# Kernel tuning notes

Measured on AMD Instinct MI355X. Metric: run time of the kernel, lower is better.

## Reference

```python
import jax, jax.numpy as jnp
import numpy as np

B, S, D = 1, 2048, 2048
H, KVH = 32, 8
HD = D // H          # 64
N_REP = H // KVH     # 4
ROPE_THETA = 10000.0
NEG = -1e9


def setup_inputs() -> dict:
    key = jax.random.key(0)
    ks = jax.random.split(key, 8)
    x = jax.random.normal(ks[0], (B, S, D), dtype=jnp.float32)
    # RoPE tables: freqs_cis[t, j] = exp(i * t * theta^{-2j/HD}), j in [0, HD/2)
    inv_freq = 1.0 / (ROPE_THETA ** (jnp.arange(0, HD, 2, dtype=jnp.float32) / HD))
    angles = jnp.arange(S, dtype=jnp.float32)[:, None] * inv_freq[None, :]  # (S, HD/2)
    freqs_cos = jnp.cos(angles)
    freqs_sin = jnp.sin(angles)
    # causal additive mask (S, S)
    mask = jnp.where(jnp.tril(jnp.ones((S, S), dtype=bool)), 0.0, NEG).astype(jnp.float32)
    sc = 0.02
    wq = jax.random.normal(ks[1], (D, H * HD), dtype=jnp.float32) * sc
    wk = jax.random.normal(ks[2], (D, KVH * HD), dtype=jnp.float32) * sc
    wv = jax.random.normal(ks[3], (D, KVH * HD), dtype=jnp.float32) * sc
    wo = jax.random.normal(ks[4], (H * HD, D), dtype=jnp.float32) * sc
    fw = jax.random.normal(ks[5], (HD, HD), dtype=jnp.float32) * sc
    fb = jnp.zeros((HD,), dtype=jnp.float32)
    return {"x": x, "freqs_cos": freqs_cos, "freqs_sin": freqs_sin, "mask": mask,
            "wq": wq, "wk": wk, "wv": wv, "wo": wo, "fw": fw, "fb": fb,
            "start_pos": 0}


def _rope(t, cos, sin):
    # t: (B, S, h, HD) -> complex rotate pairs along last dim
    tr = t.reshape(*t.shape[:-1], HD // 2, 2)
    c = cos[None, :, None, :]  # (1, S, 1, HD/2)
    s = sin[None, :, None, :]
    re = tr[..., 0] * c - tr[..., 1] * s
    im = tr[..., 0] * s + tr[..., 1] * c
    return jnp.stack([re, im], axis=-1).reshape(t.shape)


def reference(x, freqs_cos, freqs_sin, mask, wq, wk, wv, wo, fw, fb, start_pos):
    b, s, _ = x.shape
    xq = (x @ wq).reshape(b, s, H, HD)
    xk = (x @ wk).reshape(b, s, KVH, HD)
    xv = (x @ wv).reshape(b, s, KVH, HD)
    xq = _rope(xq, freqs_cos, freqs_sin)
    xk = _rope(xk, freqs_cos, freqs_sin)
    # GQA: repeat kv heads (repeat_interleave on head dim)
    keys = jnp.repeat(xk, N_REP, axis=2)    # (b, s, H, HD)
    values = jnp.repeat(xv, N_REP, axis=2)
    q = xq.transpose(0, 2, 1, 3)            # (b, H, s, HD)
    k = keys.transpose(0, 2, 1, 3)
    v = values.transpose(0, 2, 1, 3)
    scores = jnp.einsum("bhqd,bhkd->bhqk", q, k) / np.sqrt(HD).astype(np.float32)
    scores = scores + mask[None, None, :, :]
    probs = jax.nn.softmax(scores.astype(jnp.float32), axis=-1).astype(q.dtype)
    out = jnp.einsum("bhqk,bhkd->bhqd", probs, v)  # (b, H, s, HD)
    # shared per-head FFN: Linear(HD, HD) + SiLU, vectorized over heads
    out = jax.nn.silu(out @ fw + fb)
    out = out.transpose(0, 2, 1, 3).reshape(b, s, H * HD)
    return out @ wo
```

## Files before the change

### kernel.cpp

```cpp
#include <hip/hip_runtime.h>
#include <stdint.h>

#define S_LEN 2048
#define DMODEL 2048
#define NH 32
#define NKV 8
#define HD 64

typedef __attribute__((ext_vector_type(8))) __bf16 bf16x8;
typedef __attribute__((ext_vector_type(4))) float f32x4;

__device__ __forceinline__ unsigned short f2bf(float f) {
    union { float f; uint32_t u; } v; v.f = f;
    uint32_t u = v.u;
    u += 0x7FFFu + ((u >> 16) & 1u);
    return (unsigned short)(u >> 16);
}

__device__ __forceinline__ uint32_t cvt_pk_bf16(float lo, float hi) {
    uint32_t r;
    asm("v_cvt_pk_bf16_f32 %0, %1, %2" : "=v"(r) : "v"(lo), "v"(hi));
    return r;
}

#define GLDS16(g, l)                                                          \
    __builtin_amdgcn_global_load_lds(                                         \
        (const __attribute__((address_space(1))) unsigned int*)(g),           \
        (__attribute__((address_space(3))) unsigned int*)(l), 16, 0, 0)

__global__ void cast_bf16_kernel(const float* __restrict__ src,
                                 unsigned short* __restrict__ dst, int n) {
    int g = (blockIdx.x * blockDim.x + threadIdx.x) * 8;
    if (g >= n) return;
    float4 a = *(const float4*)&src[g];
    float4 b = *(const float4*)&src[g + 4];
    unsigned short o[8];
    o[0] = f2bf(a.x); o[1] = f2bf(a.y); o[2] = f2bf(a.z); o[3] = f2bf(a.w);
    o[4] = f2bf(b.x); o[5] = f2bf(b.y); o[6] = f2bf(b.z); o[7] = f2bf(b.w);
    *(uint4*)&dst[g] = *(const uint4*)o;
}

__global__ void transpose_cast_kernel(const float* __restrict__ src,
                                      unsigned short* __restrict__ dst,
                                      int R, int C) {
    __shared__ float tile[32][33];
    int c0 = blockIdx.x * 32, r0 = blockIdx.y * 32;
    int tx = threadIdx.x, ty = threadIdx.y;
#pragma unroll
    for (int i = 0; i < 32; i += 8)
        tile[ty + i][tx] = src[(size_t)(r0 + ty + i) * C + c0 + tx];
    __syncthreads();
#pragma unroll
    for (int i = 0; i < 32; i += 8)
        dst[(size_t)(c0 + ty + i) * R + r0 + tx] = f2bf(tile[tx][ty + i]);
}

__global__ __launch_bounds__(256) void gemm_bt_kernel(
    const unsigned short* __restrict__ A, const unsigned short* __restrict__ BT,
    float* __restrict__ C, int M, int N, int K) {
    __shared__ unsigned short As[2][128 * 32];
    __shared__ unsigned short Bs[2][128 * 32];
    const int t = threadIdx.x;
    const int lane = t & 63, wave = t >> 6;
    const int wr = wave >> 1, wc = wave & 1;
    const int m0 = blockIdx.x * 128, n0 = blockIdx.y * 128;
    const int l15 = lane & 15, lhi = lane >> 4;
    f32x4 acc[4][4] = {};
    const unsigned short* ga = A + (size_t)(m0 + (t >> 2)) * K + (t & 3) * 8;
    const unsigned short* gb = BT + (size_t)(n0 + (t >> 2)) * K + (t & 3) * 8;

    GLDS16(ga, &As[0][t * 8]);
    GLDS16(ga + (size_t)64 * K, &As[0][t * 8 + 64 * 32]);
    GLDS16(gb, &Bs[0][t * 8]);
    GLDS16(gb + (size_t)64 * K, &Bs[0][t * 8 + 64 * 32]);
    __syncthreads();

    int cur = 0;
    for (int k0 = 0; k0 < K; k0 += 32) {
        if (k0 + 32 < K) {
            GLDS16(ga + k0 + 32, &As[cur ^ 1][t * 8]);
            GLDS16(ga + (size_t)64 * K + k0 + 32, &As[cur ^ 1][t * 8 + 64 * 32]);
            GLDS16(gb + k0 + 32, &Bs[cur ^ 1][t * 8]);
            GLDS16(gb + (size_t)64 * K + k0 + 32, &Bs[cur ^ 1][t * 8 + 64 * 32]);
        }
        bf16x8 af[4], bfr[4];
#pragma unroll
        for (int m = 0; m < 4; m++)
            af[m] = *(const bf16x8*)&As[cur][(wr * 64 + m * 16 + l15) * 32 + lhi * 8];
#pragma unroll
        for (int n = 0; n < 4; n++)
            bfr[n] = *(const bf16x8*)&Bs[cur][(wc * 64 + n * 16 + l15) * 32 + lhi * 8];
#pragma unroll
        for (int m = 0; m < 4; m++)
#pragma unroll
            for (int n = 0; n < 4; n++)
                acc[m][n] = __builtin_amdgcn_mfma_f32_16x16x32_bf16(
                    af[m], bfr[n], acc[m][n], 0, 0, 0);
        __syncthreads();
        cur ^= 1;
    }
#pragma unroll
    for (int m = 0; m < 4; m++) {
        int row = m0 + wr * 64 + m * 16 + lhi * 4;
#pragma unroll
        for (int n = 0; n < 4; n++) {
            int col = n0 + wc * 64 + n * 16 + l15;
#pragma unroll
            for (int r = 0; r < 4; r++)
                C[(size_t)(row + r) * N + col] = acc[m][n][r];
        }
    }
}

__global__ void rope_q_kernel(const float* __restrict__ Cqkv,
                              const float* __restrict__ cb,
                              const float* __restrict__ sb,
                              unsigned short* __restrict__ Q) {
    int g = blockIdx.x * 256 + threadIdx.x;
    int i = g & 31;
    int h = (g >> 5) & 31;
    int s = g >> 10;
    float2 v = *(const float2*)&Cqkv[(size_t)s * 3072 + h * 64 + 2 * i];
    float cc = cb[s * 32 + i], ss = sb[s * 32 + i];
    ushort2 o;
    o.x = f2bf(v.x * cc - v.y * ss);
    o.y = f2bf(v.x * ss + v.y * cc);
    *(ushort2*)&Q[(size_t)h * (S_LEN * HD) + s * HD + 2 * i] = o;
}

__global__ void rope_k_kernel(const float* __restrict__ Cqkv,
                              const float* __restrict__ cb,
                              const float* __restrict__ sb,
                              unsigned short* __restrict__ Kb) {
    int g = blockIdx.x * 256 + threadIdx.x;
    int i = g & 31;
    int kvh = (g >> 5) & 7;
    int s = g >> 8;
    float2 v = *(const float2*)&Cqkv[(size_t)s * 3072 + 2048 + kvh * 64 + 2 * i];
    float cc = cb[s * 32 + i], ss = sb[s * 32 + i];
    ushort2 o;
    o.x = f2bf(v.x * cc - v.y * ss);
    o.y = f2bf(v.x * ss + v.y * cc);
    *(ushort2*)&Kb[(size_t)kvh * (S_LEN * HD) + s * HD + 2 * i] = o;
}

__global__ void v_transpose_kernel(const float* __restrict__ Cqkv,
                                   unsigned short* __restrict__ VT) {
    __shared__ float tile[32][33];
    int kvh = blockIdx.z;
    int d0 = blockIdx.x * 32, s0 = blockIdx.y * 32;
    int tx = threadIdx.x, ty = threadIdx.y;
#pragma unroll
    for (int i = 0; i < 32; i += 8)
        tile[ty + i][tx] =
            Cqkv[(size_t)(s0 + ty + i) * 3072 + 2560 + kvh * 64 + d0 + tx];
    __syncthreads();
#pragma unroll
    for (int i = 0; i < 32; i += 8)
        VT[(size_t)kvh * (HD * S_LEN) + (size_t)(d0 + ty + i) * S_LEN + s0 + tx] =
            f2bf(tile[tx][ty + i]);
}

__global__ __launch_bounds__(512) void flash_kernel(
    const unsigned short* __restrict__ Q, const unsigned short* __restrict__ Kg,
    const unsigned short* __restrict__ VTg, unsigned short* __restrict__ O) {
    __shared__ unsigned short Ks[2][4096];
    __shared__ unsigned short Vs[2][4096];
    const int t = threadIdx.x, lane = t & 63, wave = t >> 6;
    const int l15 = lane & 15, lhi = lane >> 4;
    const int bid = blockIdx.x;
    const int h = bid & 31, ss = bid >> 5;
    const int qt = (ss < 8) ? ss : 23 - ss;
    const int kvh = h >> 2;
    const float cs = 0.125f * 1.44269504f;

    const int srow = t >> 3;
    const int scol = ((t & 7) * 8) ^ ((srow & 7) * 8);
    const unsigned short* gk = Kg + ((size_t)kvh * S_LEN + srow) * HD + scol;
    const unsigned short* gv = VTg + ((size_t)kvh * HD + srow) * S_LEN + scol;

    const int q0 = qt * 128;
    const int nt = 2 * qt + 2;
    const int wq = q0 + wave * 16;
    const int wqmax = wq + 15;
    const int q = wq + l15;

    const unsigned short* qp = Q + ((size_t)h * S_LEN + q) * HD + lhi * 8;
    bf16x8 qf0 = *(const bf16x8*)qp;
    bf16x8 qf1 = *(const bf16x8*)(qp + 32);

    f32x4 oacc[4] = {};
    float mrun = -1e30f, lrun = 0.f;

    GLDS16(gk, &Ks[0][t * 8]);
    GLDS16(gv, &Vs[0][t * 8]);
    __syncthreads();

    int cur = 0;
#pragma unroll 1
    for (int kt = 0; kt < nt; ++kt) {
        const int kv0 = kt * 64;
        if (kt + 1 < nt) {
            GLDS16(gk + (size_t)(kv0 + 64) * HD, &Ks[cur ^ 1][t * 8]);
            GLDS16(gv + (kv0 + 64), &Vs[cur ^ 1][t * 8]);
        }
        if (kv0 <= wqmax) {
            f32x4 sacc[4] = {};
#pragma unroll
            for (int nb = 0; nb < 4; nb++) {
                int krow = nb * 16 + l15;
                const unsigned short* kb = &Ks[cur][krow * 64];
                int sw = (krow & 7) * 8;
                bf16x8 k0v = *(const bf16x8*)&kb[(lhi * 8) ^ sw];
                bf16x8 k1v = *(const bf16x8*)&kb[(32 + lhi * 8) ^ sw];
                sacc[nb] = __builtin_amdgcn_mfma_f32_16x16x32_bf16(k0v, qf0, sacc[nb], 0, 0, 0);
                sacc[nb] = __builtin_amdgcn_mfma_f32_16x16x32_bf16(k1v, qf1, sacc[nb], 0, 0, 0);
            }
            float pv[4][4];
            float rm = -1e30f;
            if (kv0 + 63 <= wq) {
#pragma unroll
                for (int nb = 0; nb < 4; nb++)
#pragma unroll
                    for (int r = 0; r < 4; r++) {
                        float sv = sacc[nb][r];
                        pv[nb][r] = sv;
                        rm = fmaxf(rm, sv);
                    }
            } else {
#pragma unroll
                for (int nb = 0; nb < 4; nb++) {
                    int kvb = kv0 + nb * 16 + lhi * 4;
#pragma unroll
                    for (int r = 0; r < 4; r++) {
                        float sv = (kvb + r <= q) ? sacc[nb][r] : -1e30f;
                        pv[nb][r] = sv;
                        rm = fmaxf(rm, sv);
                    }
                }
            }
            rm = fmaxf(rm, __shfl_xor(rm, 16));
            rm = fmaxf(rm, __shfl_xor(rm, 32));
            rm *= cs;
            if (!__all(rm - mrun <= 8.f)) {
                float mnew = fmaxf(mrun, rm);
                float sc = exp2f(mrun - mnew);
                mrun = mnew;
                lrun *= sc;
#pragma unroll
                for (int db = 0; db < 4; db++) oacc[db] *= sc;
            }
            float rs = 0.f;
#pragma unroll
            for (int nb = 0; nb < 4; nb++)
#pragma unroll
                for (int r = 0; r < 4; r++) {
                    float e = exp2f(fmaf(pv[nb][r], cs, -mrun));
                    pv[nb][r] = e;
                    rs += e;
                }
            rs += __shfl_xor(rs, 16);
            rs += __shfl_xor(rs, 32);
            lrun += rs;
            uint32_t pka[4], pkb[4];
#pragma unroll
            for (int nb = 0; nb < 4; nb++) {
                pka[nb] = cvt_pk_bf16(pv[nb][0], pv[nb][1]);
                pkb[nb] = cvt_pk_bf16(pv[nb][2], pv[nb][3]);
            }
            const bool selB = ((lhi >> 1) & 1);
            const bool hiR = (lhi & 1);
            const bool sendA = ((lhi ^ (lhi >> 1)) & 1);
#pragma unroll
            for (int ks = 0; ks < 2; ks++) {
                uint32_t A0 = selB ? pka[2 * ks + 1] : pka[2 * ks];
                uint32_t A1 = selB ? pkb[2 * ks + 1] : pkb[2 * ks];
                uint32_t W0 = selB ? pka[2 * ks] : pka[2 * ks + 1];
                uint32_t W1 = selB ? pkb[2 * ks] : pkb[2 * ks + 1];
                uint32_t B0 = __shfl_xor((int)W0, 32);
                uint32_t B1 = __shfl_xor((int)W1, 32);
                uint32_t S0 = sendA ? A0 : B0, S1 = sendA ? A1 : B1;
                uint32_t R0 = __shfl_xor((int)S0, 16);
                uint32_t R1 = __shfl_xor((int)S1, 16);
                uint32_t F0 = hiR ? R0 : (selB ? B0 : A0);
                uint32_t F1 = hiR ? R1 : (selB ? B1 : A1);
                uint32_t F2 = hiR ? (selB ? A0 : B0) : R0;
                uint32_t F3 = hiR ? (selB ? A1 : B1) : R1;
                uint4 fu = {F0, F1, F2, F3};
                bf16x8 pfrag = *(const bf16x8*)&fu;
#pragma unroll
                for (int db = 0; db < 4; db++) {
                    int vrow = db * 16 + l15;
                    bf16x8 vf = *(const bf16x8*)&Vs[cur][vrow * 64 + ((ks * 32 + lhi * 8) ^ ((vrow & 7) * 8))];
                    oacc[db] = __builtin_amdgcn_mfma_f32_16x16x32_bf16(vf, pfrag, oacc[db], 0, 0, 0);
                }
            }
        }
        __syncthreads();
        cur ^= 1;
    }
    float rinv = 1.f / lrun;
#pragma unroll
    for (int db = 0; db < 4; db++) {
        uint32_t o0 = cvt_pk_bf16(oacc[db][0] * rinv, oacc[db][1] * rinv);
        uint32_t o1 = cvt_pk_bf16(oacc[db][2] * rinv, oacc[db][3] * rinv);
        uint2 ov = {o0, o1};
        *(uint2*)&O[((size_t)h * S_LEN + q) * HD + db * 16 + lhi * 4] = ov;
    }
}

__global__ __launch_bounds__(256) void fw_silu_kernel(
    const unsigned short* __restrict__ AT, const unsigned short* __restrict__ fwT,
    const float* __restrict__ fb, unsigned short* __restrict__ h2) {
    const int t = threadIdx.x, lane = t & 63, wave = t >> 6;
    const int l15 = lane & 15, lhi = lane >> 4;
    const int r0 = blockIdx.x * 64 + wave * 16;
    const unsigned short* ap = AT + (size_t)(r0 + l15) * HD + lhi * 8;
    bf16x8 a0 = *(const bf16x8*)ap;
    bf16x8 a1 = *(const bf16x8*)(ap + 32);
    f32x4 acc[4] = {};
#pragma unroll
    for (int nb = 0; nb < 4; nb++) {
        const unsigned short* bp = fwT + (size_t)(nb * 16 + l15) * HD + lhi * 8;
        bf16x8 b0 = *(const bf16x8*)bp;
        bf16x8 b1 = *(const bf16x8*)(bp + 32);
        acc[nb] = __builtin_amdgcn_mfma_f32_16x16x32_bf16(a0, b0, acc[nb], 0, 0, 0);
        acc[nb] = __builtin_amdgcn_mfma_f32_16x16x32_bf16(a1, b1, acc[nb], 0, 0, 0);
    }
#pragma unroll
    for (int nb = 0; nb < 4; nb++) {
        int col = nb * 16 + l15;
        float bias = fb[col];
#pragma unroll
        for (int r = 0; r < 4; r++) {
            int row = r0 + lhi * 4 + r;
            int s = row & (S_LEN - 1), hh = row >> 11;
            float x = acc[nb][r] + bias;
            float sg = 1.f / (1.f + exp2f(-x * 1.44269504f));
            h2[(size_t)s * DMODEL + hh * HD + col] = f2bf(x * sg);
        }
    }
}

extern "C" void kernel_launch(void* const* d_in, const int* in_sizes, int n_in,
                              void* d_out, int out_size, void* d_ws, size_t ws_size,
                              hipStream_t stream) {
    const float* x = (const float*)d_in[0];
    const float* fcos = (const float*)d_in[1];
    const float* fsin = (const float*)d_in[2];
    const float* wq = (const float*)d_in[4];
    const float* wk = (const float*)d_in[5];
    const float* wv = (const float*)d_in[6];
    const float* wo = (const float*)d_in[7];
    const float* fw = (const float*)d_in[8];
    const float* fb = (const float*)d_in[9];
    float* out = (float*)d_out;

    char* ws = (char*)d_ws;
    size_t off = 0;
    auto alloc = [&](size_t bytes) {
        void* p = ws + off;
        off += (bytes + 255) & ~(size_t)255;
        return p;
    };
    unsigned short* wqkvT = (unsigned short*)alloc((size_t)3072 * 2048 * 2);
    unsigned short* woT   = (unsigned short*)alloc((size_t)2048 * 2048 * 2);
    unsigned short* fwT   = (unsigned short*)alloc((size_t)64 * 64 * 2);
    float*          Cqkv  = (float*)alloc((size_t)2048 * 3072 * 4);
    unsigned short* Qb    = (unsigned short*)alloc((size_t)NH * S_LEN * HD * 2);
    unsigned short* Kb    = (unsigned short*)alloc((size_t)NKV * S_LEN * HD * 2);
    unsigned short* VT    = (unsigned short*)alloc((size_t)NKV * HD * S_LEN * 2);
    unsigned short* xb    = (unsigned short*)alloc((size_t)2048 * 2048 * 2);
    unsigned short* attn = (unsigned short*)Cqkv;
    unsigned short* h2 = xb;

    dim3 tb(32, 8);
    cast_bf16_kernel<<<2048, 256, 0, stream>>>(x, xb, 2048 * 2048);
    transpose_cast_kernel<<<dim3(64, 64), tb, 0, stream>>>(wq, wqkvT, 2048, 2048);
    transpose_cast_kernel<<<dim3(16, 64), tb, 0, stream>>>(wk, wqkvT + (size_t)2048 * 2048, 2048, 512);
    transpose_cast_kernel<<<dim3(16, 64), tb, 0, stream>>>(wv, wqkvT + (size_t)2560 * 2048, 2048, 512);
    transpose_cast_kernel<<<dim3(64, 64), tb, 0, stream>>>(wo, woT, 2048, 2048);
    transpose_cast_kernel<<<dim3(2, 2), tb, 0, stream>>>(fw, fwT, 64, 64);

    gemm_bt_kernel<<<dim3(16, 24), 256, 0, stream>>>(xb, wqkvT, Cqkv, 2048, 3072, 2048);

    rope_q_kernel<<<8192, 256, 0, stream>>>(Cqkv, fcos, fsin, Qb);
    rope_k_kernel<<<2048, 256, 0, stream>>>(Cqkv, fcos, fsin, Kb);
    v_transpose_kernel<<<dim3(2, 64, 8), tb, 0, stream>>>(Cqkv, VT);

    flash_kernel<<<512, 512, 0, stream>>>(Qb, Kb, VT, attn);

    fw_silu_kernel<<<1024, 256, 0, stream>>>(attn, fwT, fb, h2);

    gemm_bt_kernel<<<dim3(16, 16), 256, 0, stream>>>(h2, woT, out, 2048, 2048, 2048);
}
```

Measured before the change: 192.6 us.

## Split-K output GEMM, smaller flash q-tiles, fold softmax scale into Q

The output projection GEMM now uses split-K over two halves of K. The partial sums go to a scratch buffer and a new add kernel combines them, so the 256-block launch gets more blocks. The flash kernel moves from 128-row q-tiles with 512 threads to 64-row q-tiles with 256 threads, using a new grouped zigzag tile order. It drops the per-wave early skip and defers the cross-lane row-sum reduction to the end. The softmax scale is folded into Q during RoPE, removing a multiply per score, at the cost of an extra kernel launch and extra fp32 memory traffic for the split-K partials.

After: 187.9 us. -2.4%, faster.

```diff
diff --git a/kernel.cpp b/kernel.cpp
--- a/kernel.cpp
+++ b/kernel.cpp
@@ -57,31 +57,34 @@
 
 __global__ __launch_bounds__(256) void gemm_bt_kernel(
     const unsigned short* __restrict__ A, const unsigned short* __restrict__ BT,
-    float* __restrict__ C, int M, int N, int K) {
+    float* __restrict__ C0, float* __restrict__ C1, int M, int N,
+    int Kstride, int Klen) {
     __shared__ unsigned short As[2][128 * 32];
     __shared__ unsigned short Bs[2][128 * 32];
     const int t = threadIdx.x;
     const int lane = t & 63, wave = t >> 6;
     const int wr = wave >> 1, wc = wave & 1;
     const int m0 = blockIdx.x * 128, n0 = blockIdx.y * 128;
+    const int koff = blockIdx.z * Klen;
+    float* __restrict__ C = blockIdx.z ? C1 : C0;
     const int l15 = lane & 15, lhi = lane >> 4;
     f32x4 acc[4][4] = {};
-    const unsigned short* ga = A + (size_t)(m0 + (t >> 2)) * K + (t & 3) * 8;
-    const unsigned short* gb = BT + (size_t)(n0 + (t >> 2)) * K + (t & 3) * 8;
+    const unsigned short* ga = A + (size_t)(m0 + (t >> 2)) * Kstride + koff + (t & 3) * 8;
+    const unsigned short* gb = BT + (size_t)(n0 + (t >> 2)) * Kstride + koff + (t & 3) * 8;
 
     GLDS16(ga, &As[0][t * 8]);
-    GLDS16(ga + (size_t)64 * K, &As[0][t * 8 + 64 * 32]);
+    GLDS16(ga + (size_t)64 * Kstride, &As[0][t * 8 + 64 * 32]);
     GLDS16(gb, &Bs[0][t * 8]);
-    GLDS16(gb + (size_t)64 * K, &Bs[0][t * 8 + 64 * 32]);
+    GLDS16(gb + (size_t)64 * Kstride, &Bs[0][t * 8 + 64 * 32]);
     __syncthreads();
 
     int cur = 0;
-    for (int k0 = 0; k0 < K; k0 += 32) {
-        if (k0 + 32 < K) {
+    for (int k0 = 0; k0 < Klen; k0 += 32) {
+        if (k0 + 32 < Klen) {
             GLDS16(ga + k0 + 32, &As[cur ^ 1][t * 8]);
-            GLDS16(ga + (size_t)64 * K + k0 + 32, &As[cur ^ 1][t * 8 + 64 * 32]);
+            GLDS16(ga + (size_t)64 * Kstride + k0 + 32, &As[cur ^ 1][t * 8 + 64 * 32]);
             GLDS16(gb + k0 + 32, &Bs[cur ^ 1][t * 8]);
-            GLDS16(gb + (size_t)64 * K + k0 + 32, &Bs[cur ^ 1][t * 8 + 64 * 32]);
+            GLDS16(gb + (size_t)64 * Kstride + k0 + 32, &Bs[cur ^ 1][t * 8 + 64 * 32]);
         }
         bf16x8 af[4], bfr[4];
 #pragma unroll
@@ -112,10 +115,21 @@
     }
 }
 
+__global__ void add_f32_kernel(float* __restrict__ out,
+                               const float* __restrict__ p1, int n4) {
+    int g = blockIdx.x * blockDim.x + threadIdx.x;
+    if (g >= n4) return;
+    float4 a = *(const float4*)&out[g * 4];
+    float4 b = *(const float4*)&p1[g * 4];
+    a.x += b.x; a.y += b.y; a.z += b.z; a.w += b.w;
+    *(float4*)&out[g * 4] = a;
+}
+
 __global__ void rope_q_kernel(const float* __restrict__ Cqkv,
                               const float* __restrict__ cb,
                               const float* __restrict__ sb,
                               unsigned short* __restrict__ Q) {
+    const float CS = 0.125f * 1.44269504f;
     int g = blockIdx.x * 256 + threadIdx.x;
     int i = g & 31;
     int h = (g >> 5) & 31;
@@ -123,8 +137,8 @@
     float2 v = *(const float2*)&Cqkv[(size_t)s * 3072 + h * 64 + 2 * i];
     float cc = cb[s * 32 + i], ss = sb[s * 32 + i];
     ushort2 o;
-    o.x = f2bf(v.x * cc - v.y * ss);
-    o.y = f2bf(v.x * ss + v.y * cc);
+    o.x = f2bf((v.x * cc - v.y * ss) * CS);
+    o.y = f2bf((v.x * ss + v.y * cc) * CS);
     *(ushort2*)&Q[(size_t)h * (S_LEN * HD) + s * HD + 2 * i] = o;
 }
 
@@ -161,7 +175,7 @@
             f2bf(tile[tx][ty + i]);
 }
 
-__global__ __launch_bounds__(512) void flash_kernel(
+__global__ __launch_bounds__(256) void flash_kernel(
     const unsigned short* __restrict__ Q, const unsigned short* __restrict__ Kg,
     const unsigned short* __restrict__ VTg, unsigned short* __restrict__ O) {
     __shared__ unsigned short Ks[2][4096];
@@ -169,20 +183,20 @@
     const int t = threadIdx.x, lane = t & 63, wave = t >> 6;
     const int l15 = lane & 15, lhi = lane >> 4;
     const int bid = blockIdx.x;
-    const int h = bid & 31, ss = bid >> 5;
-    const int qt = (ss < 8) ? ss : 23 - ss;
+    const int h = bid & 31;
+    const int u = bid >> 5;
+    const int grp = u >> 3, pos = u & 7;
+    const int qt = (grp & 1) ? (grp * 8 + 7 - pos) : (grp * 8 + pos);
     const int kvh = h >> 2;
-    const float cs = 0.125f * 1.44269504f;
 
     const int srow = t >> 3;
     const int scol = ((t & 7) * 8) ^ ((srow & 7) * 8);
     const unsigned short* gk = Kg + ((size_t)kvh * S_LEN + srow) * HD + scol;
     const unsigned short* gv = VTg + ((size_t)kvh * HD + srow) * S_LEN + scol;
 
-    const int q0 = qt * 128;
-    const int nt = 2 * qt + 2;
+    const int q0 = qt * 64;
+    const int nt = qt + 1;
     const int wq = q0 + wave * 16;
-    const int wqmax = wq + 15;
     const int q = wq + l15;
 
     const unsigned short* qp = Q + ((size_t)h * S_LEN + q) * HD + lhi * 8;
@@ -193,7 +207,9 @@
     float mrun = -1e30f, lrun = 0.f;
 
     GLDS16(gk, &Ks[0][t * 8]);
+    GLDS16(gk + (size_t)32 * HD, &Ks[0][t * 8 + 2048]);
     GLDS16(gv, &Vs[0][t * 8]);
+    GLDS16(gv + (size_t)32 * S_LEN, &Vs[0][t * 8 + 2048]);
     __syncthreads();
 
     int cur = 0;
@@ -202,103 +218,102 @@
         const int kv0 = kt * 64;
         if (kt + 1 < nt) {
             GLDS16(gk + (size_t)(kv0 + 64) * HD, &Ks[cur ^ 1][t * 8]);
+            GLDS16(gk + (size_t)(kv0 + 96) * HD, &Ks[cur ^ 1][t * 8 + 2048]);
             GLDS16(gv + (kv0 + 64), &Vs[cur ^ 1][t * 8]);
-        }
-        if (kv0 <= wqmax) {
-            f32x4 sacc[4] = {};
+            GLDS16(gv + (size_t)32 * S_LEN + (kv0 + 64), &Vs[cur ^ 1][t * 8 + 2048]);
+        }
+        f32x4 sacc[4] = {};
+#pragma unroll
+        for (int nb = 0; nb < 4; nb++) {
+            int krow = nb * 16 + l15;
+            const unsigned short* kb = &Ks[cur][krow * 64];
+            int sw = (krow & 7) * 8;
+            bf16x8 k0v = *(const bf16x8*)&kb[(lhi * 8) ^ sw];
+            bf16x8 k1v = *(const bf16x8*)&kb[(32 + lhi * 8) ^ sw];
+            sacc[nb] = __builtin_amdgcn_mfma_f32_16x16x32_bf16(k0v, qf0, sacc[nb], 0, 0, 0);
+            sacc[nb] = __builtin_amdgcn_mfma_f32_16x16x32_bf16(k1v, qf1, sacc[nb], 0, 0, 0);
+        }
+        float pv[4][4];
+        float lm = -1e30f;
+        if (kv0 + 63 <= wq) {
+#pragma unroll
+            for (int nb = 0; nb < 4; nb++)
+#pragma unroll
+                for (int r = 0; r < 4; r++) {
+                    float sv = sacc[nb][r];
+                    pv[nb][r] = sv;
+                    lm = fmaxf(lm, sv);
+                }
+        } else {
 #pragma unroll
             for (int nb = 0; nb < 4; nb++) {
-                int krow = nb * 16 + l15;
-                const unsigned short* kb = &Ks[cur][krow * 64];
-                int sw = (krow & 7) * 8;
-                bf16x8 k0v = *(const bf16x8*)&kb[(lhi * 8) ^ sw];
-                bf16x8 k1v = *(const bf16x8*)&kb[(32 + lhi * 8) ^ sw];
-                sacc[nb] = __builtin_amdgcn_mfma_f32_16x16x32_bf16(k0v, qf0, sacc[nb], 0, 0, 0);
-                sacc[nb] = __builtin_amdgcn_mfma_f32_16x16x32_bf16(k1v, qf1, sacc[nb], 0, 0, 0);
-            }
-            float pv[4][4];
-            float rm = -1e30f;
-            if (kv0 + 63 <= wq) {
-#pragma unroll
-                for (int nb = 0; nb < 4; nb++)
-#pragma unroll
-                    for (int r = 0; r < 4; r++) {
-                        float sv = sacc[nb][r];
-                        pv[nb][r] = sv;
-                        rm = fmaxf(rm, sv);
-                    }
-            } else {
-#pragma unroll
-                for (int nb = 0; nb < 4; nb++) {
-                    int kvb = kv0 + nb * 16 + lhi * 4;
-#pragma unroll
-                    for (int r = 0; r < 4; r++) {
-                        float sv = (kvb + r <= q) ? sacc[nb][r] : -1e30f;
-                        pv[nb][r] = sv;
-                        rm = fmaxf(rm, sv);
-                    }
+                int kvb = kv0 + nb * 16 + lhi * 4;
+#pragma unroll
+                for (int r = 0; r < 4; r++) {
+                    float sv = (kvb + r <= q) ? sacc[nb][r] : -1e30f;
+                    pv[nb][r] = sv;
+                    lm = fmaxf(lm, sv);
                 }
             }
-            rm = fmaxf(rm, __shfl_xor(rm, 16));
+        }
+        if (!__all(lm - mrun <= 8.f)) {
+            float rm = fmaxf(lm, __shfl_xor(lm, 16));
             rm = fmaxf(rm, __shfl_xor(rm, 32));
-            rm *= cs;
-            if (!__all(rm - mrun <= 8.f)) {
-                float mnew = fmaxf(mrun, rm);
-                float sc = exp2f(mrun - mnew);
-                mrun = mnew;
-                lrun *= sc;
-#pragma unroll
-                for (int db = 0; db < 4; db++) oacc[db] *= sc;
+            float mnew = fmaxf(mrun, rm);
+            float sc = exp2f(mrun - mnew);
+            mrun = mnew;
+            lrun *= sc;
+#pragma unroll
+            for (int db = 0; db < 4; db++) oacc[db] *= sc;
+        }
+        float rs = 0.f;
+#pragma unroll
+        for (int nb = 0; nb < 4; nb++)
+#pragma unroll
+            for (int r = 0; r < 4; r++) {
+                float e = exp2f(pv[nb][r] - mrun);
+                pv[nb][r] = e;
+                rs += e;
             }
-            float rs = 0.f;
-#pragma unroll
-            for (int nb = 0; nb < 4; nb++)
-#pragma unroll
-                for (int r = 0; r < 4; r++) {
-                    float e = exp2f(fmaf(pv[nb][r], cs, -mrun));
-                    pv[nb][r] = e;
-                    rs += e;
-                }
-            rs += __shfl_xor(rs, 16);
-            rs += __shfl_xor(rs, 32);
-            lrun += rs;
-            uint32_t pka[4], pkb[4];
-#pragma unroll
-            for (int nb = 0; nb < 4; nb++) {
-                pka[nb] = cvt_pk_bf16(pv[nb][0], pv[nb][1]);
-                pkb[nb] = cvt_pk_bf16(pv[nb][2], pv[nb][3]);
-            }
-            const bool selB = ((lhi >> 1) & 1);
-            const bool hiR = (lhi & 1);
-            const bool sendA = ((lhi ^ (lhi >> 1)) & 1);
-#pragma unroll
-            for (int ks = 0; ks < 2; ks++) {
-                uint32_t A0 = selB ? pka[2 * ks + 1] : pka[2 * ks];
-                uint32_t A1 = selB ? pkb[2 * ks + 1] : pkb[2 * ks];
-                uint32_t W0 = selB ? pka[2 * ks] : pka[2 * ks + 1];
-                uint32_t W1 = selB ? pkb[2 * ks] : pkb[2 * ks + 1];
-                uint32_t B0 = __shfl_xor((int)W0, 32);
-                uint32_t B1 = __shfl_xor((int)W1, 32);
-                uint32_t S0 = sendA ? A0 : B0, S1 = sendA ? A1 : B1;
-                uint32_t R0 = __shfl_xor((int)S0, 16);
-                uint32_t R1 = __shfl_xor((int)S1, 16);
-                uint32_t F0 = hiR ? R0 : (selB ? B0 : A0);
-                uint32_t F1 = hiR ? R1 : (selB ? B1 : A1);
-                uint32_t F2 = hiR ? (selB ? A0 : B0) : R0;
-                uint32_t F3 = hiR ? (selB ? A1 : B1) : R1;
-                uint4 fu = {F0, F1, F2, F3};
-                bf16x8 pfrag = *(const bf16x8*)&fu;
-#pragma unroll
-                for (int db = 0; db < 4; db++) {
-                    int vrow = db * 16 + l15;
-                    bf16x8 vf = *(const bf16x8*)&Vs[cur][vrow * 64 + ((ks * 32 + lhi * 8) ^ ((vrow & 7) * 8))];
-                    oacc[db] = __builtin_amdgcn_mfma_f32_16x16x32_bf16(vf, pfrag, oacc[db], 0, 0, 0);
-                }
+        lrun += rs;
+        uint32_t pka[4], pkb[4];
+#pragma unroll
+        for (int nb = 0; nb < 4; nb++) {
+            pka[nb] = cvt_pk_bf16(pv[nb][0], pv[nb][1]);
+            pkb[nb] = cvt_pk_bf16(pv[nb][2], pv[nb][3]);
+        }
+        const bool selB = ((lhi >> 1) & 1);
+        const bool hiR = (lhi & 1);
+        const bool sendA = ((lhi ^ (lhi >> 1)) & 1);
+#pragma unroll
+        for (int ks = 0; ks < 2; ks++) {
+            uint32_t A0 = selB ? pka[2 * ks + 1] : pka[2 * ks];
+            uint32_t A1 = selB ? pkb[2 * ks + 1] : pkb[2 * ks];
+            uint32_t W0 = selB ? pka[2 * ks] : pka[2 * ks + 1];
+            uint32_t W1 = selB ? pkb[2 * ks] : pkb[2 * ks + 1];
+            uint32_t B0 = __shfl_xor((int)W0, 32);
+            uint32_t B1 = __shfl_xor((int)W1, 32);
+            uint32_t S0 = sendA ? A0 : B0, S1 = sendA ? A1 : B1;
+            uint32_t R0 = __shfl_xor((int)S0, 16);
+            uint32_t R1 = __shfl_xor((int)S1, 16);
+            uint32_t F0 = hiR ? R0 : (selB ? B0 : A0);
+            uint32_t F1 = hiR ? R1 : (selB ? B1 : A1);
+            uint32_t F2 = hiR ? (selB ? A0 : B0) : R0;
+            uint32_t F3 = hiR ? (selB ? A1 : B1) : R1;
+            uint4 fu = {F0, F1, F2, F3};
+            bf16x8 pfrag = *(const bf16x8*)&fu;
+#pragma unroll
+            for (int db = 0; db < 4; db++) {
+                int vrow = db * 16 + l15;
+                bf16x8 vf = *(const bf16x8*)&Vs[cur][vrow * 64 + ((ks * 32 + lhi * 8) ^ ((vrow & 7) * 8))];
+                oacc[db] = __builtin_amdgcn_mfma_f32_16x16x32_bf16(vf, pfrag, oacc[db], 0, 0, 0);
             }
         }
         __syncthreads();
         cur ^= 1;
     }
+    lrun += __shfl_xor(lrun, 16);
+    lrun += __shfl_xor(lrun, 32);
     float rinv = 1.f / lrun;
 #pragma unroll
     for (int db = 0; db < 4; db++) {
@@ -372,6 +387,7 @@
     unsigned short* VT    = (unsigned short*)alloc((size_t)NKV * HD * S_LEN * 2);
     unsigned short* xb    = (unsigned short*)alloc((size_t)2048 * 2048 * 2);
     unsigned short* attn = (unsigned short*)Cqkv;
+    float* P1 = (float*)((char*)Cqkv + (size_t)NH * S_LEN * HD * 2);
     unsigned short* h2 = xb;
 
     dim3 tb(32, 8);
@@ -382,15 +398,18 @@
     transpose_cast_kernel<<<dim3(64, 64), tb, 0, stream>>>(wo, woT, 2048, 2048);
     transpose_cast_kernel<<<dim3(2, 2), tb, 0, stream>>>(fw, fwT, 64, 64);
 
-    gemm_bt_kernel<<<dim3(16, 24), 256, 0, stream>>>(xb, wqkvT, Cqkv, 2048, 3072, 2048);
+    gemm_bt_kernel<<<dim3(16, 24, 1), 256, 0, stream>>>(xb, wqkvT, Cqkv, nullptr,
+                                                        2048, 3072, 2048, 2048);
 
     rope_q_kernel<<<8192, 256, 0, stream>>>(Cqkv, fcos, fsin, Qb);
     rope_k_kernel<<<2048, 256, 0, stream>>>(Cqkv, fcos, fsin, Kb);
     v_transpose_kernel<<<dim3(2, 64, 8), tb, 0, stream>>>(Cqkv, VT);
 
-    flash_kernel<<<512, 512, 0, stream>>>(Qb, Kb, VT, attn);
+    flash_kernel<<<1024, 256, 0, stream>>>(Qb, Kb, VT, attn);
 
     fw_silu_kernel<<<1024, 256, 0, stream>>>(attn, fwT, fb, h2);
 
-    gemm_bt_kernel<<<dim3(16, 16), 256, 0, stream>>>(h2, woT, out, 2048, 2048, 2048);
-}
+    gemm_bt_kernel<<<dim3(16, 16, 2), 256, 0, stream>>>(h2, woT, out, P1,
+                                                        2048, 2048, 2048, 1024);
+    add_f32_kernel<<<4096, 256, 0, stream>>>(out, P1, 1048576);
+}
```
